# Kernel tuning notes

Hardware: AMD Instinct MI355X
Metric: run time of the kernel (lower is better)

Reference implementation:

```python
import jax, jax.numpy as jnp
import numpy as np

# ---- fan-beam geometry config (uniform path: no pmatrix, uniform SID/SDD/angle/offcenter) ----
SID = 750.0          # source-to-isocenter distance (mm)
SDD = 1250.0         # source-to-detector distance (mm)
VIEWS = 128          # number of projection angles
NDET = 512           # detector element count
DET_ELT = 1.2        # detector element size (mm)
DET_OFF = 0.0        # detector offcenter (mm)
START_ANGLE = 0.0    # degrees
TOTAL_ANGLE = 360.0  # degrees
IMG_DIM = 256        # image is IMG_DIM x IMG_DIM
PIX = 1.0            # pixel size (mm)
STEP = 1.0           # fpjStepSize: ray sampling step (mm)
R = IMG_DIM * PIX * np.sqrt(2.0) / 2.0   # half image diagonal: ray segment to sample
NS = int(np.ceil(2.0 * R / STEP)) + 1    # samples per ray (static)


def _sample_points():
    # Per-view source / detector geometry; rays sampled from t = SID-R to SID+R.
    beta = jnp.asarray(np.deg2rad(START_ANGLE + TOTAL_ANGLE * np.arange(VIEWS) / VIEWS),
                       jnp.float32)                                    # [V]
    cb, sb = jnp.cos(beta), jnp.sin(beta)
    src = SID * jnp.stack([cb, sb], -1)                                 # [V,2] source position
    det0 = src - SDD * jnp.stack([cb, sb], -1)                          # [V,2] detector center
    eu = jnp.stack([-sb, cb], -1)                                       # [V,2] detector tangent
    u = (jnp.arange(NDET, dtype=jnp.float32) - (NDET - 1) / 2.0) * DET_ELT + DET_OFF  # [N]
    det = det0[:, None, :] + u[None, :, None] * eu[:, None, :]          # [V,N,2]
    d = det - src[:, None, :]
    d = d / jnp.linalg.norm(d, axis=-1, keepdims=True)                  # unit ray directions
    t = SID - R + STEP * jnp.arange(NS, dtype=jnp.float32)              # [NS]
    pts = src[:, None, None, :] + t[None, None, :, None] * d[:, :, None, :]  # [V,N,NS,2]
    return pts


def setup_inputs() -> dict:
    key = jax.random.key(0)
    x = jax.random.uniform(key, (2, IMG_DIM, IMG_DIM), dtype=jnp.float32)  # attenuation image batch
    return {"x": x}


def reference(x):
    # Ray-driven fan-beam forward projection: line integral via bilinear sampling.
    pts = _sample_points()                      # [V,N,NS,2] world coords (mm)
    px, py = pts[..., 0], pts[..., 1]
    jx = px / PIX + (IMG_DIM - 1) / 2.0         # continuous column index
    iy = (IMG_DIM - 1) / 2.0 - py / PIX         # continuous row index (y up)
    j0f = jnp.floor(jx)
    i0f = jnp.floor(iy)
    fj = jx - j0f
    fi = iy - i0f
    i0 = i0f.astype(jnp.int32)
    j0 = j0f.astype(jnp.int32)

    def gather(ii, jj):
        valid = (ii >= 0) & (ii < IMG_DIM) & (jj >= 0) & (jj < IMG_DIM)
        ic = jnp.clip(ii, 0, IMG_DIM - 1)
        jc = jnp.clip(jj, 0, IMG_DIM - 1)
        return x[:, ic, jc] * valid[None].astype(x.dtype)   # [B,V,N,NS]

    v00 = gather(i0, j0)
    v01 = gather(i0, j0 + 1)
    v10 = gather(i0 + 1, j0)
    v11 = gather(i0 + 1, j0 + 1)
    interp = (v00 * (1 - fi) * (1 - fj) + v01 * (1 - fi) * fj
              + v10 * fi * (1 - fj) + v11 * fi * fj)        # [B,V,N,NS]
    sinogram = interp.sum(-1) * STEP                        # [B,V,N]
    return sinogram
```

## Files before the change

### kernel.cpp

```cpp
#include <hip/hip_runtime.h>
#include <hip/hip_fp16.h>
#include <math.h>

constexpr int   VIEWS = 128;
constexpr int   NDET  = 512;
constexpr int   IMG   = 256;
constexpr int   BATCH = 2;
constexpr float SID_F = 750.0f;
constexpr float SDD_F = 1250.0f;
constexpr float DET_ELT = 1.2f;
constexpr float DET_OFF = 0.0f;
constexpr float STEP  = 1.0f;
constexpr int   NS = 364;
constexpr float T0 = (float)(750.0 - 181.01933598375618);

constexpr int CSTR   = 261;
constexpr int NE_T   = 131;
constexpr int NE_B   = 130;
constexpr int BLO_B  = 129;
constexpr int SPLIT  = 130;
constexpr int TILE_DW = 34192;

typedef _Float16 h2 __attribute__((ext_vector_type(2)));
using v2h = decltype(__builtin_amdgcn_cvt_pkrtz(0.0f, 0.0f));

__device__ __forceinline__ unsigned pk16(float lo, float hi) {
    return __builtin_bit_cast(unsigned, __builtin_amdgcn_cvt_pkrtz(lo, hi));
}

__device__ __forceinline__ float band_loop(const unsigned* __restrict__ tb,
                                           int lo, int hi, int chunk,
                                           float dx, float ndy,
                                           float cx3, float cy3) {
    float acc = 0.0f;
    const int start = lo + chunk;
    const int iters = max(0, (hi - start + 2) / 2);
    float sfv = (float)start;
#pragma unroll 4
    for (int k = 0; k < iters; ++k) {
        const float jx2 = fmaf(sfv, dx, cx3);
        const float iy2 = fmaf(sfv, ndy, cy3);
        sfv += 2.0f;
        const int jp = (int)jx2;
        const int ip = (int)iy2;
        const float fj = jx2 - (float)jp;
        const float fi = iy2 - (float)ip;
        const int addr = ip * CSTR + jp;
        const unsigned Lu = tb[addr];
        const unsigned Hu = tb[addr + 1];
        const h2 L = __builtin_bit_cast(h2, Lu);
        const h2 H = __builtin_bit_cast(h2, Hu);
        const h2 fj2 = __builtin_bit_cast(h2, __builtin_amdgcn_cvt_pkrtz(fj, fj));
        const h2 r = fj2 * (H - L) + L;
#if __has_builtin(__builtin_amdgcn_fdot2)
        const h2 wv = __builtin_bit_cast(h2, __builtin_amdgcn_cvt_pkrtz(1.0f - fi, fi));
        acc = __builtin_amdgcn_fdot2(__builtin_bit_cast(v2h, r),
                                     __builtin_bit_cast(v2h, wv), acc, false);
#else
        acc = fmaf(fi, (float)r.y - (float)r.x, acc + (float)r.x);
#endif
    }
    return acc;
}

__global__ __launch_bounds__(1024) void fanbeam_band(const float* __restrict__ img,
                                                     float* __restrict__ out) {
    __shared__ __align__(16) unsigned tile[TILE_DW];
    __shared__ float red[1024];
    const int tid  = threadIdx.x;
    const int bb   = blockIdx.x;
    const int band = bb & 1;
    const int bv   = bb >> 1;
    const int v = bv & (VIEWS - 1);
    const int b = bv >> 7;
    const float* __restrict__ src = img + b * IMG * IMG;
    const bool bandT = (band == 0);

    for (int k = tid; k < TILE_DW / 4; k += 1024)
        reinterpret_cast<uint4*>(tile)[k] = uint4{0u, 0u, 0u, 0u};
    __syncthreads();

    const int NF = bandT ? 129 : 128;
    const int E0 = bandT ? 2 : 0;
    const int R0 = bandT ? 0 : 127;
    for (int k = tid; k < NF * 64; k += 1024) {
        const int er = k >> 6;
        const int c  = (k & 63) << 2;
        const int e  = E0 + er;
        const int r0 = R0 + er;
        const float4 a = *reinterpret_cast<const float4*>(src + (r0 << 8) + c);
        const float4 d = *reinterpret_cast<const float4*>(src + ((r0 + 1) << 8) + c);
        const int base = e * CSTR + c + 2;
        tile[base + 0] = pk16(a.x, d.x);
        tile[base + 1] = pk16(a.y, d.y);
        tile[base + 2] = pk16(a.z, d.z);
        tile[base + 3] = pk16(a.w, d.w);
    }
    for (int k = tid; k < 256; k += 1024) {
        if (bandT) {
            const unsigned hb = (unsigned)__half_as_ushort(__float2half(src[k]));
            tile[1 * CSTR + k + 2] = hb << 16;
        } else {
            const unsigned lb = (unsigned)__half_as_ushort(__float2half(src[(255 << 8) + k]));
            tile[128 * CSTR + k + 2] = lb;
        }
    }
    __syncthreads();

    const int n     = tid & (NDET - 1);
    const int chunk = tid >> 9;
    const float beta = (float)((double)v * 0.049087385212340517);
    const float cb = cosf(beta);
    const float sb = sinf(beta);
    const float u  = ((float)n - 255.5f) * DET_ELT + DET_OFF;
    float dx = fmaf(-u, sb, -SDD_F * cb);
    float dy = fmaf( u, cb, -SDD_F * sb);
    const float rinv = rsqrtf(fmaf(dx, dx, dy * dy));
    dx *= rinv;
    dy *= rinv;
    const float ndy = -dy;
    const float sx = SID_F * cb;
    const float sy = SID_F * sb;
    const float cx3 = fmaf(T0, dx,  sx + 127.5f + 2.0f);
    const float cy3 = fmaf(T0, ndy, 127.5f - sy + 2.0f);

    const float invx = 1.0f / dx;
    const float invy = 1.0f / dy;
    const float ta = (-128.75f - sx) * invx, tb2 = (128.75f - sx) * invx;
    const float tc = (-128.75f - sy) * invy, td = (128.75f - sy) * invy;
    const float tmin = fmaxf(fmaxf(fminf(ta, tb2), fminf(tc, td)), T0);
    const float tmax = fminf(fminf(fmaxf(ta, tb2), fmaxf(tc, td)), T0 + (float)(NS - 1));
    int slo = (int)ceilf(tmin - T0);
    int shi = (int)floorf(tmax - T0);
    slo = max(slo, 0);
    shi = min(shi, NS - 1);

    float zf = (cy3 - (float)SPLIT) * invy;
    zf = fminf(fmaxf(zf, -1.0e6f), 1.0e6f);
    const int zc  = (int)ceilf(zf);
    const int zfl = (int)floorf(zf);

    int lo_, hi_;
    if (bandT) {
        if (ndy > 0.0f)      { lo_ = slo; hi_ = min(shi, zc - 1); }
        else if (ndy < 0.0f) { lo_ = max(slo, zfl + 1); hi_ = shi; }
        else                 { lo_ = (cy3 < (float)SPLIT) ? slo : 1;
                               hi_ = (cy3 < (float)SPLIT) ? shi : 0; }
    } else {
        if (ndy > 0.0f)      { lo_ = max(slo, zc); hi_ = shi; }
        else if (ndy < 0.0f) { lo_ = slo; hi_ = min(shi, zfl); }
        else                 { lo_ = (cy3 < (float)SPLIT) ? 1 : slo;
                               hi_ = (cy3 < (float)SPLIT) ? 0 : shi; }
    }
    const float cy3loc = bandT ? cy3 : (cy3 - (float)BLO_B);
    const float acc = band_loop(tile, lo_, hi_, chunk, dx, ndy, cx3, cy3loc);

    red[tid] = acc;
    __syncthreads();
    if (tid < 512) {
        const float r = (red[tid] + red[tid + 512]) * STEP;
        unsafeAtomicAdd(&out[bv * 512 + tid], r);
    }
}

extern "C" void kernel_launch(void* const* d_in, const int* in_sizes, int n_in,
                              void* d_out, int out_size, void* d_ws, size_t ws_size,
                              hipStream_t stream) {
    const float* x = (const float*)d_in[0];
    float* out = (float*)d_out;
    hipMemsetAsync(out, 0, (size_t)out_size * sizeof(float), stream);
    fanbeam_band<<<2 * BATCH * VIEWS, 1024, 0, stream>>>(x, out);
}
```

Before: 81.47 us.

## Store fp16 tile row-major with column pairs instead of row-pair packing

```diff
diff --git a/kernel.cpp b/kernel.cpp
--- a/kernel.cpp
+++ b/kernel.cpp
@@ -14,12 +14,10 @@
 constexpr int   NS = 364;
 constexpr float T0 = (float)(750.0 - 181.01933598375618);
 
-constexpr int CSTR   = 261;
-constexpr int NE_T   = 131;
-constexpr int NE_B   = 130;
-constexpr int BLO_B  = 129;
-constexpr int SPLIT  = 130;
-constexpr int TILE_DW = 34192;
+constexpr int TWSTR   = 131;
+constexpr int TILE_DW = 132 * TWSTR;
+constexpr int SPLIT   = 130;
+constexpr int BLO_B   = 129;
 
 typedef _Float16 h2 __attribute__((ext_vector_type(2)));
 using v2h = decltype(__builtin_amdgcn_cvt_pkrtz(0.0f, 0.0f));
@@ -28,7 +26,7 @@
     return __builtin_bit_cast(unsigned, __builtin_amdgcn_cvt_pkrtz(lo, hi));
 }
 
-__device__ __forceinline__ float band_loop(const unsigned* __restrict__ tb,
+__device__ __forceinline__ float band_loop(const unsigned* __restrict__ tile32,
                                            int lo, int hi, int chunk,
                                            float dx, float ndy,
                                            float cx3, float cy3) {
@@ -45,9 +43,16 @@
         const int ip = (int)iy2;
         const float fj = jx2 - (float)jp;
         const float fi = iy2 - (float)ip;
-        const int addr = ip * CSTR + jp;
-        const unsigned Lu = tb[addr];
-        const unsigned Hu = tb[addr + 1];
+        const int w = ip * TWSTR + (jp >> 1);
+        const unsigned w0 = tile32[w];
+        const unsigned w1 = tile32[w + 1];
+        const unsigned w2 = tile32[w + TWSTR];
+        const unsigned w3 = tile32[w + TWSTR + 1];
+        const unsigned sh = (unsigned)jp << 4;
+        const unsigned ptop = __builtin_amdgcn_alignbit(w1, w0, sh);
+        const unsigned pbot = __builtin_amdgcn_alignbit(w3, w2, sh);
+        const unsigned Lu = __builtin_amdgcn_perm(pbot, ptop, 0x05040100u);
+        const unsigned Hu = __builtin_amdgcn_perm(pbot, ptop, 0x07060302u);
         const h2 L = __builtin_bit_cast(h2, Lu);
         const h2 H = __builtin_bit_cast(h2, Hu);
         const h2 fj2 = __builtin_bit_cast(h2, __builtin_amdgcn_cvt_pkrtz(fj, fj));
@@ -63,8 +68,8 @@
     return acc;
 }
 
-__global__ __launch_bounds__(1024) void fanbeam_band(const float* __restrict__ img,
-                                                     float* __restrict__ out) {
+__global__ __launch_bounds__(1024) void fanbeam_band2(const float* __restrict__ img,
+                                                      float* __restrict__ out) {
     __shared__ __align__(16) unsigned tile[TILE_DW];
     __shared__ float red[1024];
     const int tid  = threadIdx.x;
@@ -80,30 +85,16 @@
         reinterpret_cast<uint4*>(tile)[k] = uint4{0u, 0u, 0u, 0u};
     __syncthreads();
 
-    const int NF = bandT ? 129 : 128;
-    const int E0 = bandT ? 2 : 0;
-    const int R0 = bandT ? 0 : 127;
-    for (int k = tid; k < NF * 64; k += 1024) {
+    const int NR = bandT ? 130 : 129;
+    const int RT = bandT ? 2 : 0;
+    const int RI = bandT ? 0 : 127;
+    for (int k = tid; k < NR * 64; k += 1024) {
         const int er = k >> 6;
         const int c  = (k & 63) << 2;
-        const int e  = E0 + er;
-        const int r0 = R0 + er;
-        const float4 a = *reinterpret_cast<const float4*>(src + (r0 << 8) + c);
-        const float4 d = *reinterpret_cast<const float4*>(src + ((r0 + 1) << 8) + c);
-        const int base = e * CSTR + c + 2;
-        tile[base + 0] = pk16(a.x, d.x);
-        tile[base + 1] = pk16(a.y, d.y);
-        tile[base + 2] = pk16(a.z, d.z);
-        tile[base + 3] = pk16(a.w, d.w);
-    }
-    for (int k = tid; k < 256; k += 1024) {
-        if (bandT) {
-            const unsigned hb = (unsigned)__half_as_ushort(__float2half(src[k]));
-            tile[1 * CSTR + k + 2] = hb << 16;
-        } else {
-            const unsigned lb = (unsigned)__half_as_ushort(__float2half(src[(255 << 8) + k]));
-            tile[128 * CSTR + k + 2] = lb;
-        }
+        const float4 a = *reinterpret_cast<const float4*>(src + ((RI + er) << 8) + c);
+        const int base = (RT + er) * TWSTR + (c >> 1) + 1;
+        tile[base]     = pk16(a.x, a.y);
+        tile[base + 1] = pk16(a.z, a.w);
     }
     __syncthreads();
 
@@ -169,5 +160,5 @@
     const float* x = (const float*)d_in[0];
     float* out = (float*)d_out;
     hipMemsetAsync(out, 0, (size_t)out_size * sizeof(float), stream);
-    fanbeam_band<<<2 * BATCH * VIEWS, 1024, 0, stream>>>(x, out);
+    fanbeam_band2<<<2 * BATCH * VIEWS, 1024, 0, stream>>>(x, out);
 }
```

Measured after the change: 80.07 us. Within noise of the previous version (-1.7%).
